# Performance work log

Hardware: AMD Instinct MI355X
Metric: run time of the kernel (lower is better)

Reference implementation:

```python
import jax, jax.numpy as jnp
import numpy as np

B, SRC = 32, 1024
SEQ_LEN, CONTEXT_LEN, D_MODEL, VOCAB = 128, 5, 512, 32000


def setup_inputs() -> dict:
    key = jax.random.key(0)
    k1, k2, k3, k4, k5, k6 = jax.random.split(key, 6)
    x = jax.random.randint(k1, (B, SRC), 0, VOCAB, dtype=jnp.int64 if jax.config.jax_enable_x64 else jnp.int32)
    yc = jax.random.randint(k2, (B, SEQ_LEN * CONTEXT_LEN), 0, VOCAB, dtype=x.dtype)
    F_emb = jax.random.normal(k3, (VOCAB, D_MODEL), dtype=jnp.float32) * 0.02
    G_emb = jax.random.normal(k4, (VOCAB, D_MODEL), dtype=jnp.float32) * 0.02
    fan_in = CONTEXT_LEN * D_MODEL
    P_w = jax.random.uniform(k5, (fan_in, D_MODEL), dtype=jnp.float32,
                             minval=-1.0, maxval=1.0) * (fan_in ** -0.5)
    P_b = jnp.zeros((D_MODEL,), dtype=jnp.float32)
    return {"x": x, "yc": yc, "F_emb": F_emb, "G_emb": G_emb, "P_w": P_w, "P_b": P_b}


def reference(x, yc, F_emb, G_emb, P_w, P_b):
    # padding mask from source tokens: 1.0 where token == 0
    mask = (x == 0).astype(jnp.float32)                      # [B, SRC]
    xe = F_emb[x]                                            # [B, SRC, D]
    yce = G_emb[yc].reshape(-1, SEQ_LEN, CONTEXT_LEN * D_MODEL)  # [B, SEQ, C*D]
    py = jnp.einsum('bsk,kd->bsd', yce, P_w) + P_b           # Dense P(y): [B, SEQ, D]
    a = jnp.einsum('bxd,bsd->bxs', xe, py)                   # [B, SRC, SEQ]
    a = a + mask[:, :, None] * -1e9                          # mask padded source rows
    a = jnp.transpose(a, (0, 2, 1))                          # [B, SEQ, SRC]
    a = jax.nn.softmax(a, axis=-1)
    out = jnp.einsum('bsx,bxd->bsd', a, xe)                  # [B, SEQ, D]
    return (out, a)
```

## Files before the change

kernel.cpp:

```cpp
#include <hip/hip_runtime.h>
#include <hip/hip_bf16.h>
#include <stdint.h>

#define BATCH 32
#define SRCN 1024
#define SEQL 128
#define CTXN 5
#define DMOD 512

typedef __attribute__((ext_vector_type(8))) short short8;
typedef __attribute__((ext_vector_type(4))) float floatx4;

typedef __attribute__((address_space(3))) void lds_t;
typedef __attribute__((address_space(1))) void glb_t;

__device__ __forceinline__ void gload_lds16(const void* g, void* l) {
    __builtin_amdgcn_global_load_lds((const glb_t*)g, (lds_t*)l, 16, 0, 0);
}

__device__ __forceinline__ ushort f2b(float f) {
    __hip_bfloat16 h = __float2bfloat16(f);
    return *reinterpret_cast<ushort*>(&h);
}

#define LSLOT(m, sg) ((((m) << 3) | ((sg) ^ ((m) & 7))) << 3)

__global__ __launch_bounds__(256) void k_prep(
    const int* __restrict__ yc, const float* __restrict__ G,
    ushort* __restrict__ yce,
    const float* __restrict__ Pw, ushort* __restrict__ Pwt)
{
    const int tid = threadIdx.x;
    if (blockIdx.x < 4096) {
        const int r = blockIdx.x;
        const int b = r >> 7, s = r & 127;
        for (int i = tid; i < 640; i += 256) {
            const int c = i >> 7;
            const int tok = yc[b * (SEQL * CTXN) + s * CTXN + c];
            const float4 v = *(const float4*)(G + (size_t)tok * DMOD + (i & 127) * 4);
            ushort4 o;
            o.x = f2b(v.x); o.y = f2b(v.y); o.z = f2b(v.z); o.w = f2b(v.w);
            *(ushort4*)(yce + (size_t)r * 2560 + i * 4) = o;
        }
    } else {
        __shared__ float t[64][68];
        const int bid = blockIdx.x - 4096;
        const int k0 = (bid % 40) * 64, n0 = (bid / 40) * 64;
        #pragma unroll
        for (int it = 0; it < 4; ++it) {
            const int c = tid + it * 256;
            const int kr = c >> 4, c4 = c & 15;
            const float4 v = *(const float4*)(Pw + (size_t)(k0 + kr) * DMOD + n0 + c4 * 4);
            t[kr][c4 * 4 + 0] = v.x; t[kr][c4 * 4 + 1] = v.y;
            t[kr][c4 * 4 + 2] = v.z; t[kr][c4 * 4 + 3] = v.w;
        }
        __syncthreads();
        #pragma unroll
        for (int it = 0; it < 2; ++it) {
            const int c = tid + it * 256;
            const int n = c >> 3, seg = c & 7;
            ushort4 o0, o1;
            o0.x = f2b(t[seg * 8 + 0][n]); o0.y = f2b(t[seg * 8 + 1][n]);
            o0.z = f2b(t[seg * 8 + 2][n]); o0.w = f2b(t[seg * 8 + 3][n]);
            o1.x = f2b(t[seg * 8 + 4][n]); o1.y = f2b(t[seg * 8 + 5][n]);
            o1.z = f2b(t[seg * 8 + 6][n]); o1.w = f2b(t[seg * 8 + 7][n]);
            ushort* dst = Pwt + (size_t)(n0 + n) * 2560 + k0 + seg * 8;
            *(ushort4*)dst = o0; *(ushort4*)(dst + 4) = o1;
        }
    }
}

__global__ __launch_bounds__(256) void k_gemm_py(
    const ushort* __restrict__ yce, const ushort* __restrict__ pwt,
    float* __restrict__ part)
{
    __shared__ ushort As[16 * 512];
    __shared__ ushort Bs[8 * 512];
    const int f = blockIdx.x;
    const int mlo = f & 7;
    const int n   = (f >> 3) & 7;
    const int mhi = (f >> 6) & 3;
    const int ks  = f >> 8;
    const int m = mlo | (mhi << 3);
    const int tid = threadIdx.x;
    const int w = tid >> 6, lane = tid & 63;
    const int l15 = lane & 15, q = lane >> 4;
    const int wm = w >> 1, wn = w & 1;
    const int m0 = m * 128, n0 = n * 64, koff = ks * 640;

    const int sr = lane >> 3;
    const int ssg = ((lane & 7) ^ sr) * 8;

    const ushort* Abase = yce + (size_t)(m0 + sr) * 2560 + koff + ssg;
    const ushort* Bbase = pwt + (size_t)(n0 + sr) * 2560 + koff + ssg;

    floatx4 acc[4][2];
    #pragma unroll
    for (int mi = 0; mi < 4; ++mi)
        #pragma unroll
        for (int ni = 0; ni < 2; ++ni)
            acc[mi][ni] = (floatx4){0.f, 0.f, 0.f, 0.f};

    for (int kk = 0; kk < 640; kk += 64) {
        __syncthreads();
        #pragma unroll
        for (int i = 0; i < 4; ++i) {
            const int cc = w * 4 + i;
            gload_lds16(Abase + (size_t)(cc * 8) * 2560 + kk, (void*)(As + cc * 512));
        }
        #pragma unroll
        for (int i = 0; i < 2; ++i) {
            const int cc = w * 2 + i;
            gload_lds16(Bbase + (size_t)(cc * 8) * 2560 + kk, (void*)(Bs + cc * 512));
        }
        __syncthreads();
        #pragma unroll
        for (int s2 = 0; s2 < 2; ++s2) {
            const int sg = s2 * 4 + q;
            short8 af[4], bf[2];
            #pragma unroll
            for (int mi = 0; mi < 4; ++mi)
                af[mi] = *(const short8*)(As + LSLOT(wm * 64 + mi * 16 + l15, sg));
            #pragma unroll
            for (int ni = 0; ni < 2; ++ni)
                bf[ni] = *(const short8*)(Bs + LSLOT(wn * 32 + ni * 16 + l15, sg));
            #pragma unroll
            for (int mi = 0; mi < 4; ++mi)
                #pragma unroll
                for (int ni = 0; ni < 2; ++ni)
                    acc[mi][ni] = __builtin_amdgcn_mfma_f32_16x16x32_bf16(
                        af[mi], bf[ni], acc[mi][ni], 0, 0, 0);
        }
    }

    float* dst = part + (size_t)ks * (4096LL * DMOD);
    #pragma unroll
    for (int ni = 0; ni < 2; ++ni) {
        const int col = n0 + wn * 32 + ni * 16 + l15;
        #pragma unroll
        for (int mi = 0; mi < 4; ++mi) {
            const int row0 = m0 + wm * 64 + mi * 16 + q * 4;
            #pragma unroll
            for (int r = 0; r < 4; ++r)
                dst[(size_t)(row0 + r) * DMOD + col] = acc[mi][ni][r];
        }
    }
}

__global__ __launch_bounds__(256) void k_red4(
    const float* __restrict__ part, const float* __restrict__ Pb,
    ushort* __restrict__ py)
{
    const long long SL = 4096LL * DMOD;
    const int i = blockIdx.x * 256 + threadIdx.x;
    const float4 a = *(const float4*)(part + (size_t)i * 4);
    const float4 b = *(const float4*)(part + SL + (size_t)i * 4);
    const float4 c = *(const float4*)(part + 2 * SL + (size_t)i * 4);
    const float4 d = *(const float4*)(part + 3 * SL + (size_t)i * 4);
    const float4 bias = *(const float4*)(Pb + ((i * 4) & 511));
    ushort4 o;
    o.x = f2b(a.x + b.x + c.x + d.x + bias.x);
    o.y = f2b(a.y + b.y + c.y + d.y + bias.y);
    o.z = f2b(a.z + b.z + c.z + d.z + bias.z);
    o.w = f2b(a.w + b.w + c.w + d.w + bias.w);
    *(ushort4*)(py + (size_t)i * 4) = o;
}

__global__ __launch_bounds__(256) void k_xe2(
    const int* __restrict__ x, const float* __restrict__ F,
    ushort* __restrict__ xe, ushort* __restrict__ xet)
{
    __shared__ ushort t[64][72];
    const int z = blockIdx.z;
    const int x0 = blockIdx.x * 64, d0 = blockIdx.y * 64;
    const int tid = threadIdx.x;
    #pragma unroll
    for (int it = 0; it < 4; ++it) {
        const int c = tid + it * 256;
        const int row = c >> 4, seg = c & 15;
        const int tok = x[z * SRCN + x0 + row];
        const float4 v = *(const float4*)(F + (size_t)tok * DMOD + d0 + seg * 4);
        ushort4 o;
        o.x = f2b(v.x); o.y = f2b(v.y); o.z = f2b(v.z); o.w = f2b(v.w);
        *(ushort4*)&t[row][seg * 4] = o;
        *(ushort4*)(xe + (size_t)(z * SRCN + x0 + row) * DMOD + d0 + seg * 4) = o;
    }
    __syncthreads();
    #pragma unroll
    for (int it = 0; it < 2; ++it) {
        const int c = tid + it * 256;
        const int d = c >> 3, seg = c & 7;
        ushort4 o0, o1;
        o0.x = t[seg * 8 + 0][d]; o0.y = t[seg * 8 + 1][d];
        o0.z = t[seg * 8 + 2][d]; o0.w = t[seg * 8 + 3][d];
        o1.x = t[seg * 8 + 4][d]; o1.y = t[seg * 8 + 5][d];
        o1.z = t[seg * 8 + 6][d]; o1.w = t[seg * 8 + 7][d];
        ushort* dst = xet + (size_t)(z * DMOD + d0 + d) * SRCN + x0 + seg * 8;
        *(ushort4*)dst = o0; *(ushort4*)(dst + 4) = o1;
    }
}

__global__ __launch_bounds__(256) void k_gemm_sc(
    const ushort* __restrict__ py, const int* __restrict__ x,
    const ushort* __restrict__ xe, float* __restrict__ a_out)
{
    __shared__ ushort As[16 * 512];
    __shared__ ushort Bs[8 * 512];
    const int f = blockIdx.x;
    const int g = f >> 3;
    const int b = ((g & 3) << 3) | (f & 7);
    const int n = g >> 2;
    const int tid = threadIdx.x;
    const int w = tid >> 6, lane = tid & 63;
    const int l15 = lane & 15, q = lane >> 4;
    const int wm = w >> 1, wn = w & 1;
    const int n0 = n * 64;

    const int sr = lane >> 3;
    const int ssg = ((lane & 7) ^ sr) * 8;

    const ushort* Abase = py + (size_t)(b * SEQL + sr) * DMOD + ssg;
    const ushort* Bbase = xe + (size_t)(b * SRCN + n0 + sr) * DMOD + ssg;

    floatx4 acc[4][2];
    #pragma unroll
    for (int mi = 0; mi < 4; ++mi)
        #pragma unroll
        for (int ni = 0; ni < 2; ++ni)
            acc[mi][ni] = (floatx4){0.f, 0.f, 0.f, 0.f};

    for (int kk = 0; kk < DMOD; kk += 64) {
        __syncthreads();
        #pragma unroll
        for (int i = 0; i < 4; ++i) {
            const int cc = w * 4 + i;
            gload_lds16(Abase + (size_t)(cc * 8) * DMOD + kk, (void*)(As + cc * 512));
        }
        #pragma unroll
        for (int i = 0; i < 2; ++i) {
            const int cc = w * 2 + i;
            gload_lds16(Bbase + (size_t)(cc * 8) * DMOD + kk, (void*)(Bs + cc * 512));
        }
        __syncthreads();
        #pragma unroll
        for (int s2 = 0; s2 < 2; ++s2) {
            const int sg = s2 * 4 + q;
            short8 af[4], bf[2];
            #pragma unroll
            for (int mi = 0; mi < 4; ++mi)
                af[mi] = *(const short8*)(As + LSLOT(wm * 64 + mi * 16 + l15, sg));
            #pragma unroll
            for (int ni = 0; ni < 2; ++ni)
                bf[ni] = *(const short8*)(Bs + LSLOT(wn * 32 + ni * 16 + l15, sg));
            #pragma unroll
            for (int mi = 0; mi < 4; ++mi)
                #pragma unroll
                for (int ni = 0; ni < 2; ++ni)
                    acc[mi][ni] = __builtin_amdgcn_mfma_f32_16x16x32_bf16(
                        af[mi], bf[ni], acc[mi][ni], 0, 0, 0);
        }
    }

    #pragma unroll
    for (int ni = 0; ni < 2; ++ni) {
        const int col = n0 + wn * 32 + ni * 16 + l15;
        const float msk = (x[b * SRCN + col] == 0) ? -1e9f : 0.0f;
        #pragma unroll
        for (int mi = 0; mi < 4; ++mi) {
            const int row0 = wm * 64 + mi * 16 + q * 4;
            #pragma unroll
            for (int r = 0; r < 4; ++r)
                a_out[((size_t)b * SEQL + row0 + r) * SRCN + col] = acc[mi][ni][r] + msk;
        }
    }
}

__global__ __launch_bounds__(256) void k_softmax(
    float* __restrict__ a, ushort* __restrict__ abf)
{
    const int row = blockIdx.x;
    float* p = a + (size_t)row * SRCN;
    ushort* pb = abf + (size_t)row * SRCN;
    const int tid = threadIdx.x;
    const int wave = tid >> 6, lane = tid & 63;

    float4 v = *(const float4*)(p + tid * 4);

    float mx = fmaxf(fmaxf(v.x, v.y), fmaxf(v.z, v.w));
    #pragma unroll
    for (int off = 32; off > 0; off >>= 1)
        mx = fmaxf(mx, __shfl_down(mx, off, 64));
    __shared__ float redm[4];
    if (lane == 0) redm[wave] = mx;
    __syncthreads();
    mx = fmaxf(fmaxf(redm[0], redm[1]), fmaxf(redm[2], redm[3]));

    const float e0 = __expf(v.x - mx);
    const float e1 = __expf(v.y - mx);
    const float e2 = __expf(v.z - mx);
    const float e3 = __expf(v.w - mx);

    float sm = e0 + e1 + e2 + e3;
    #pragma unroll
    for (int off = 32; off > 0; off >>= 1)
        sm += __shfl_down(sm, off, 64);
    __shared__ float reds[4];
    if (lane == 0) reds[wave] = sm;
    __syncthreads();
    sm = reds[0] + reds[1] + reds[2] + reds[3];

    const float inv = 1.0f / sm;
    float4 o;
    o.x = e0 * inv; o.y = e1 * inv; o.z = e2 * inv; o.w = e3 * inv;
    *(float4*)(p + tid * 4) = o;
    ushort4 ob;
    ob.x = f2b(o.x); ob.y = f2b(o.y); ob.z = f2b(o.z); ob.w = f2b(o.w);
    *(ushort4*)(pb + tid * 4) = ob;
}

__global__ __launch_bounds__(256) void k_gemm_out(
    const ushort* __restrict__ abf, const ushort* __restrict__ xet,
    float* __restrict__ outp)
{
    __shared__ ushort As[2 * 8 * 512];
    __shared__ ushort Bs[2 * 8 * 512];
    const int f = blockIdx.x;
    const int g = f >> 3;
    const int b = ((g & 3) << 3) | (f & 7);
    const int h = g >> 2;
    const int m = h & 1, n = h >> 1;
    const int tid = threadIdx.x;
    const int w = tid >> 6, lane = tid & 63;
    const int l15 = lane & 15, q = lane >> 4;
    const int wm = w >> 1, wn = w & 1;
    const int m0 = m * 64, n0 = n * 64;

    const int sr = lane >> 3;
    const int ssg = ((lane & 7) ^ sr) * 8;

    const ushort* Abase = abf + (size_t)(b * SEQL + m0 + sr) * SRCN + ssg;
    const ushort* Bbase = xet + (size_t)(b * DMOD + n0 + sr) * SRCN + ssg;

    floatx4 acc[2][2];
    #pragma unroll
    for (int mi = 0; mi < 2; ++mi)
        #pragma unroll
        for (int ni = 0; ni < 2; ++ni)
            acc[mi][ni] = (floatx4){0.f, 0.f, 0.f, 0.f};

    for (int kk = 0; kk < SRCN; kk += 128) {
        __syncthreads();
        #pragma unroll
        for (int sub = 0; sub < 2; ++sub) {
            #pragma unroll
            for (int i = 0; i < 2; ++i) {
                const int cc = w * 2 + i;
                gload_lds16(Abase + (size_t)(cc * 8) * SRCN + kk + sub * 64,
                            (void*)(As + sub * 4096 + cc * 512));
                gload_lds16(Bbase + (size_t)(cc * 8) * SRCN + kk + sub * 64,
                            (void*)(Bs + sub * 4096 + cc * 512));
            }
        }
        __syncthreads();
        #pragma unroll
        for (int sub = 0; sub < 2; ++sub) {
            #pragma unroll
            for (int s2 = 0; s2 < 2; ++s2) {
                const int sg = s2 * 4 + q;
                short8 af[2], bf[2];
                #pragma unroll
                for (int mi = 0; mi < 2; ++mi)
                    af[mi] = *(const short8*)(As + sub * 4096 + LSLOT(wm * 32 + mi * 16 + l15, sg));
                #pragma unroll
                for (int ni = 0; ni < 2; ++ni)
                    bf[ni] = *(const short8*)(Bs + sub * 4096 + LSLOT(wn * 32 + ni * 16 + l15, sg));
                #pragma unroll
                for (int mi = 0; mi < 2; ++mi)
                    #pragma unroll
                    for (int ni = 0; ni < 2; ++ni)
                        acc[mi][ni] = __builtin_amdgcn_mfma_f32_16x16x32_bf16(
                            af[mi], bf[ni], acc[mi][ni], 0, 0, 0);
            }
        }
    }

    #pragma unroll
    for (int ni = 0; ni < 2; ++ni) {
        const int col = n0 + wn * 32 + ni * 16 + l15;
        #pragma unroll
        for (int mi = 0; mi < 2; ++mi) {
            const int row0 = m0 + wm * 32 + mi * 16 + q * 4;
            #pragma unroll
            for (int r = 0; r < 4; ++r)
                outp[((size_t)b * SEQL + row0 + r) * DMOD + col] = acc[mi][ni][r];
        }
    }
}

extern "C" void kernel_launch(void* const* d_in, const int* in_sizes, int n_in,
                              void* d_out, int out_size, void* d_ws, size_t ws_size,
                              hipStream_t stream)
{
    const int*   x    = (const int*)d_in[0];
    const int*   yc   = (const int*)d_in[1];
    const float* Femb = (const float*)d_in[2];
    const float* Gemb = (const float*)d_in[3];
    const float* Pw   = (const float*)d_in[4];
    const float* Pb   = (const float*)d_in[5];

    float* out_p = (float*)d_out;
    float* a_p   = out_p + (size_t)BATCH * SEQL * DMOD;

    char* ws = (char*)d_ws;
    ushort* yce  = (ushort*)(ws);
    ushort* pwt  = (ushort*)(ws + 20971520);
    float*  part = (float*) (ws + 23592960);
    ushort* xe   = (ushort*)(ws);
    ushort* xet  = (ushort*)(ws + 33554432);
    ushort* py   = (ushort*)(ws + 67108864);
    ushort* abf  = (ushort*)(ws + 71303168);

    dim3 blk(256);
    k_prep<<<dim3(4416), blk, 0, stream>>>(yc, Gemb, yce, Pw, pwt);

    k_gemm_py<<<dim3(1024), blk, 0, stream>>>(yce, pwt, part);
    k_red4<<<dim3(2048), blk, 0, stream>>>(part, Pb, py);

    k_xe2<<<dim3(16, 8, 32), blk, 0, stream>>>(x, Femb, xe, xet);

    k_gemm_sc<<<dim3(512), blk, 0, stream>>>(py, x, xe, a_p);
    k_softmax<<<dim3(4096), blk, 0, stream>>>(a_p, abf);
    k_gemm_out<<<dim3(512), blk, 0, stream>>>(abf, xet, out_p);
}
```

Baseline: 221.4 us.

## Merge gather kernels, drop split-K partials, fuse bias into py GEMM epilogue

The xe/xet embedding gather and transpose now run in the same launch as the yce gather and Pw transpose, so one kernel covers all preprocessing. The py GEMM drops its 4-way split-K with fp32 partial buffers and the separate reduction kernel. It now computes full-K 64x64 tiles with two 64-wide K sub-slabs per barrier and adds the bias in its epilogue before converting to bf16. The aim is to cut a launch and the 32MB partial write/read traffic. In exchange each GEMM block does a longer serial K loop with a smaller tile and less reuse per block, and the workspace layout is reshuffled so abf aliases yce.

```diff
diff --git a/kernel.cpp b/kernel.cpp
--- a/kernel.cpp
+++ b/kernel.cpp
@@ -25,14 +25,18 @@
 
 #define LSLOT(m, sg) ((((m) << 3) | ((sg) ^ ((m) & 7))) << 3)
 
-__global__ __launch_bounds__(256) void k_prep(
+__global__ __launch_bounds__(256) void k_gather(
     const int* __restrict__ yc, const float* __restrict__ G,
     ushort* __restrict__ yce,
-    const float* __restrict__ Pw, ushort* __restrict__ Pwt)
-{
+    const float* __restrict__ Pw, ushort* __restrict__ Pwt,
+    const int* __restrict__ x, const float* __restrict__ F,
+    ushort* __restrict__ xe, ushort* __restrict__ xet)
+{
+    __shared__ char smem[17408];
     const int tid = threadIdx.x;
-    if (blockIdx.x < 4096) {
-        const int r = blockIdx.x;
+    const int bid = blockIdx.x;
+    if (bid < 4096) {
+        const int r = bid;
         const int b = r >> 7, s = r & 127;
         for (int i = tid; i < 640; i += 256) {
             const int c = i >> 7;
@@ -42,17 +46,17 @@
             o.x = f2b(v.x); o.y = f2b(v.y); o.z = f2b(v.z); o.w = f2b(v.w);
             *(ushort4*)(yce + (size_t)r * 2560 + i * 4) = o;
         }
-    } else {
-        __shared__ float t[64][68];
-        const int bid = blockIdx.x - 4096;
-        const int k0 = (bid % 40) * 64, n0 = (bid / 40) * 64;
+    } else if (bid < 4416) {
+        float* t = (float*)smem;
+        const int id = bid - 4096;
+        const int k0 = (id % 40) * 64, n0 = (id / 40) * 64;
         #pragma unroll
         for (int it = 0; it < 4; ++it) {
             const int c = tid + it * 256;
             const int kr = c >> 4, c4 = c & 15;
             const float4 v = *(const float4*)(Pw + (size_t)(k0 + kr) * DMOD + n0 + c4 * 4);
-            t[kr][c4 * 4 + 0] = v.x; t[kr][c4 * 4 + 1] = v.y;
-            t[kr][c4 * 4 + 2] = v.z; t[kr][c4 * 4 + 3] = v.w;
+            t[kr * 68 + c4 * 4 + 0] = v.x; t[kr * 68 + c4 * 4 + 1] = v.y;
+            t[kr * 68 + c4 * 4 + 2] = v.z; t[kr * 68 + c4 * 4 + 3] = v.w;
         }
         __syncthreads();
         #pragma unroll
@@ -60,143 +64,121 @@
             const int c = tid + it * 256;
             const int n = c >> 3, seg = c & 7;
             ushort4 o0, o1;
-            o0.x = f2b(t[seg * 8 + 0][n]); o0.y = f2b(t[seg * 8 + 1][n]);
-            o0.z = f2b(t[seg * 8 + 2][n]); o0.w = f2b(t[seg * 8 + 3][n]);
-            o1.x = f2b(t[seg * 8 + 4][n]); o1.y = f2b(t[seg * 8 + 5][n]);
-            o1.z = f2b(t[seg * 8 + 6][n]); o1.w = f2b(t[seg * 8 + 7][n]);
+            o0.x = f2b(t[(seg * 8 + 0) * 68 + n]); o0.y = f2b(t[(seg * 8 + 1) * 68 + n]);
+            o0.z = f2b(t[(seg * 8 + 2) * 68 + n]); o0.w = f2b(t[(seg * 8 + 3) * 68 + n]);
+            o1.x = f2b(t[(seg * 8 + 4) * 68 + n]); o1.y = f2b(t[(seg * 8 + 5) * 68 + n]);
+            o1.z = f2b(t[(seg * 8 + 6) * 68 + n]); o1.w = f2b(t[(seg * 8 + 7) * 68 + n]);
             ushort* dst = Pwt + (size_t)(n0 + n) * 2560 + k0 + seg * 8;
             *(ushort4*)dst = o0; *(ushort4*)(dst + 4) = o1;
         }
+    } else {
+        ushort* t = (ushort*)smem;
+        const int id = bid - 4416;
+        const int z = id >> 7;
+        const int rem = id & 127;
+        const int x0 = (rem & 15) * 64, d0 = (rem >> 4) * 64;
+        #pragma unroll
+        for (int it = 0; it < 4; ++it) {
+            const int c = tid + it * 256;
+            const int row = c >> 4, seg = c & 15;
+            const int tok = x[z * SRCN + x0 + row];
+            const float4 v = *(const float4*)(F + (size_t)tok * DMOD + d0 + seg * 4);
+            ushort4 o;
+            o.x = f2b(v.x); o.y = f2b(v.y); o.z = f2b(v.z); o.w = f2b(v.w);
+            *(ushort4*)&t[row * 72 + seg * 4] = o;
+            *(ushort4*)(xe + (size_t)(z * SRCN + x0 + row) * DMOD + d0 + seg * 4) = o;
+        }
+        __syncthreads();
+        #pragma unroll
+        for (int it = 0; it < 2; ++it) {
+            const int c = tid + it * 256;
+            const int d = c >> 3, seg = c & 7;
+            ushort4 o0, o1;
+            o0.x = t[(seg * 8 + 0) * 72 + d]; o0.y = t[(seg * 8 + 1) * 72 + d];
+            o0.z = t[(seg * 8 + 2) * 72 + d]; o0.w = t[(seg * 8 + 3) * 72 + d];
+            o1.x = t[(seg * 8 + 4) * 72 + d]; o1.y = t[(seg * 8 + 5) * 72 + d];
+            o1.z = t[(seg * 8 + 6) * 72 + d]; o1.w = t[(seg * 8 + 7) * 72 + d];
+            ushort* dst = xet + (size_t)(z * DMOD + d0 + d) * SRCN + x0 + seg * 8;
+            *(ushort4*)dst = o0; *(ushort4*)(dst + 4) = o1;
+        }
     }
 }
 
 __global__ __launch_bounds__(256) void k_gemm_py(
     const ushort* __restrict__ yce, const ushort* __restrict__ pwt,
-    float* __restrict__ part)
-{
-    __shared__ ushort As[16 * 512];
-    __shared__ ushort Bs[8 * 512];
+    const float* __restrict__ Pb, ushort* __restrict__ py)
+{
+    __shared__ ushort As[2 * 8 * 512];
+    __shared__ ushort Bs[2 * 8 * 512];
     const int f = blockIdx.x;
-    const int mlo = f & 7;
-    const int n   = (f >> 3) & 7;
-    const int mhi = (f >> 6) & 3;
-    const int ks  = f >> 8;
-    const int m = mlo | (mhi << 3);
+    const int wg = ((f & 7) << 6) | (f >> 3);
+    const int m = wg >> 3, n = wg & 7;
     const int tid = threadIdx.x;
     const int w = tid >> 6, lane = tid & 63;
     const int l15 = lane & 15, q = lane >> 4;
     const int wm = w >> 1, wn = w & 1;
-    const int m0 = m * 128, n0 = n * 64, koff = ks * 640;
+    const int m0 = m * 64, n0 = n * 64;
 
     const int sr = lane >> 3;
     const int ssg = ((lane & 7) ^ sr) * 8;
 
-    const ushort* Abase = yce + (size_t)(m0 + sr) * 2560 + koff + ssg;
-    const ushort* Bbase = pwt + (size_t)(n0 + sr) * 2560 + koff + ssg;
-
-    floatx4 acc[4][2];
-    #pragma unroll
-    for (int mi = 0; mi < 4; ++mi)
+    const ushort* Abase = yce + (size_t)(m0 + sr) * 2560 + ssg;
+    const ushort* Bbase = pwt + (size_t)(n0 + sr) * 2560 + ssg;
+
+    floatx4 acc[2][2];
+    #pragma unroll
+    for (int mi = 0; mi < 2; ++mi)
         #pragma unroll
         for (int ni = 0; ni < 2; ++ni)
             acc[mi][ni] = (floatx4){0.f, 0.f, 0.f, 0.f};
 
-    for (int kk = 0; kk < 640; kk += 64) {
-        __syncthreads();
-        #pragma unroll
-        for (int i = 0; i < 4; ++i) {
-            const int cc = w * 4 + i;
-            gload_lds16(Abase + (size_t)(cc * 8) * 2560 + kk, (void*)(As + cc * 512));
-        }
-        #pragma unroll
-        for (int i = 0; i < 2; ++i) {
-            const int cc = w * 2 + i;
-            gload_lds16(Bbase + (size_t)(cc * 8) * 2560 + kk, (void*)(Bs + cc * 512));
-        }
-        __syncthreads();
-        #pragma unroll
-        for (int s2 = 0; s2 < 2; ++s2) {
-            const int sg = s2 * 4 + q;
-            short8 af[4], bf[2];
-            #pragma unroll
-            for (int mi = 0; mi < 4; ++mi)
-                af[mi] = *(const short8*)(As + LSLOT(wm * 64 + mi * 16 + l15, sg));
-            #pragma unroll
-            for (int ni = 0; ni < 2; ++ni)
-                bf[ni] = *(const short8*)(Bs + LSLOT(wn * 32 + ni * 16 + l15, sg));
-            #pragma unroll
-            for (int mi = 0; mi < 4; ++mi)
+    for (int kk = 0; kk < 2560; kk += 128) {
+        __syncthreads();
+        #pragma unroll
+        for (int sub = 0; sub < 2; ++sub) {
+            #pragma unroll
+            for (int i = 0; i < 2; ++i) {
+                const int cc = w * 2 + i;
+                gload_lds16(Abase + (size_t)(cc * 8) * 2560 + kk + sub * 64,
+                            (void*)(As + sub * 4096 + cc * 512));
+                gload_lds16(Bbase + (size_t)(cc * 8) * 2560 + kk + sub * 64,
+                            (void*)(Bs + sub * 4096 + cc * 512));
+            }
+        }
+        __syncthreads();
+        #pragma unroll
+        for (int sub = 0; sub < 2; ++sub) {
+            #pragma unroll
+            for (int s2 = 0; s2 < 2; ++s2) {
+                const int sg = s2 * 4 + q;
+                short8 af[2], bf[2];
+                #pragma unroll
+                for (int mi = 0; mi < 2; ++mi)
+                    af[mi] = *(const short8*)(As + sub * 4096 + LSLOT(wm * 32 + mi * 16 + l15, sg));
                 #pragma unroll
                 for (int ni = 0; ni < 2; ++ni)
-                    acc[mi][ni] = __builtin_amdgcn_mfma_f32_16x16x32_bf16(
-                        af[mi], bf[ni], acc[mi][ni], 0, 0, 0);
-        }
-    }
-
-    float* dst = part + (size_t)ks * (4096LL * DMOD);
+                    bf[ni] = *(const short8*)(Bs + sub * 4096 + LSLOT(wn * 32 + ni * 16 + l15, sg));
+                #pragma unroll
+                for (int mi = 0; mi < 2; ++mi)
+                    #pragma unroll
+                    for (int ni = 0; ni < 2; ++ni)
+                        acc[mi][ni] = __builtin_amdgcn_mfma_f32_16x16x32_bf16(
+                            af[mi], bf[ni], acc[mi][ni], 0, 0, 0);
+            }
+        }
+    }
+
     #pragma unroll
     for (int ni = 0; ni < 2; ++ni) {
         const int col = n0 + wn * 32 + ni * 16 + l15;
-        #pragma unroll
-        for (int mi = 0; mi < 4; ++mi) {
-            const int row0 = m0 + wm * 64 + mi * 16 + q * 4;
+        const float bias = Pb[col];
+        #pragma unroll
+        for (int mi = 0; mi < 2; ++mi) {
+            const int row0 = m0 + wm * 32 + mi * 16 + q * 4;
             #pragma unroll
             for (int r = 0; r < 4; ++r)
-                dst[(size_t)(row0 + r) * DMOD + col] = acc[mi][ni][r];
-        }
-    }
-}
-
-__global__ __launch_bounds__(256) void k_red4(
-    const float* __restrict__ part, const float* __restrict__ Pb,
-    ushort* __restrict__ py)
-{
-    const long long SL = 4096LL * DMOD;
-    const int i = blockIdx.x * 256 + threadIdx.x;
-    const float4 a = *(const float4*)(part + (size_t)i * 4);
-    const float4 b = *(const float4*)(part + SL + (size_t)i * 4);
-    const float4 c = *(const float4*)(part + 2 * SL + (size_t)i * 4);
-    const float4 d = *(const float4*)(part + 3 * SL + (size_t)i * 4);
-    const float4 bias = *(const float4*)(Pb + ((i * 4) & 511));
-    ushort4 o;
-    o.x = f2b(a.x + b.x + c.x + d.x + bias.x);
-    o.y = f2b(a.y + b.y + c.y + d.y + bias.y);
-    o.z = f2b(a.z + b.z + c.z + d.z + bias.z);
-    o.w = f2b(a.w + b.w + c.w + d.w + bias.w);
-    *(ushort4*)(py + (size_t)i * 4) = o;
-}
-
-__global__ __launch_bounds__(256) void k_xe2(
-    const int* __restrict__ x, const float* __restrict__ F,
-    ushort* __restrict__ xe, ushort* __restrict__ xet)
-{
-    __shared__ ushort t[64][72];
-    const int z = blockIdx.z;
-    const int x0 = blockIdx.x * 64, d0 = blockIdx.y * 64;
-    const int tid = threadIdx.x;
-    #pragma unroll
-    for (int it = 0; it < 4; ++it) {
-        const int c = tid + it * 256;
-        const int row = c >> 4, seg = c & 15;
-        const int tok = x[z * SRCN + x0 + row];
-        const float4 v = *(const float4*)(F + (size_t)tok * DMOD + d0 + seg * 4);
-        ushort4 o;
-        o.x = f2b(v.x); o.y = f2b(v.y); o.z = f2b(v.z); o.w = f2b(v.w);
-        *(ushort4*)&t[row][seg * 4] = o;
-        *(ushort4*)(xe + (size_t)(z * SRCN + x0 + row) * DMOD + d0 + seg * 4) = o;
-    }
-    __syncthreads();
-    #pragma unroll
-    for (int it = 0; it < 2; ++it) {
-        const int c = tid + it * 256;
-        const int d = c >> 3, seg = c & 7;
-        ushort4 o0, o1;
-        o0.x = t[seg * 8 + 0][d]; o0.y = t[seg * 8 + 1][d];
-        o0.z = t[seg * 8 + 2][d]; o0.w = t[seg * 8 + 3][d];
-        o1.x = t[seg * 8 + 4][d]; o1.y = t[seg * 8 + 5][d];
-        o1.z = t[seg * 8 + 6][d]; o1.w = t[seg * 8 + 7][d];
-        ushort* dst = xet + (size_t)(z * DMOD + d0 + d) * SRCN + x0 + seg * 8;
-        *(ushort4*)dst = o0; *(ushort4*)(dst + 4) = o1;
+                py[(size_t)(row0 + r) * DMOD + col] = f2b(acc[mi][ni][r] + bias);
+        }
     }
 }
 
@@ -413,20 +395,16 @@
 
     char* ws = (char*)d_ws;
     ushort* yce  = (ushort*)(ws);
+    ushort* abf  = (ushort*)(ws);
     ushort* pwt  = (ushort*)(ws + 20971520);
-    float*  part = (float*) (ws + 23592960);
-    ushort* xe   = (ushort*)(ws);
-    ushort* xet  = (ushort*)(ws + 33554432);
-    ushort* py   = (ushort*)(ws + 67108864);
-    ushort* abf  = (ushort*)(ws + 71303168);
+    ushort* xe   = (ushort*)(ws + 23592960);
+    ushort* xet  = (ushort*)(ws + 57147392);
+    ushort* py   = (ushort*)(ws + 90701824);
 
     dim3 blk(256);
-    k_prep<<<dim3(4416), blk, 0, stream>>>(yc, Gemb, yce, Pw, pwt);
-
-    k_gemm_py<<<dim3(1024), blk, 0, stream>>>(yce, pwt, part);
-    k_red4<<<dim3(2048), blk, 0, stream>>>(part, Pb, py);
-
-    k_xe2<<<dim3(16, 8, 32), blk, 0, stream>>>(x, Femb, xe, xet);
+    k_gather<<<dim3(8512), blk, 0, stream>>>(yc, Gemb, yce, Pw, pwt, x, Femb, xe, xet);
+
+    k_gemm_py<<<dim3(512), blk, 0, stream>>>(yce, pwt, Pb, py);
 
     k_gemm_sc<<<dim3(512), blk, 0, stream>>>(py, x, xe, a_p);
     k_softmax<<<dim3(4096), blk, 0, stream>>>(a_p, abf);
```

Result: faster. 211.7 us (-4.4%).

## Merge xe gather into prep kernel and halve py GEMM split-K

Applied to the files above, without the earlier changes.

Folds the F-embedding gather and transpose into the same launch as the yc gather and Pw transpose, using wider 128-row tiles with an XOR-swizzled LDS layout and 16-byte transposed stores. The py GEMM goes from 4-way to 2-way split-K, which halves the partial-sum traffic and simplifies the reduction. Workspace buffers are rearranged so xe no longer aliases yce. It also adds smem token caching and odd padding for the Pw transpose. The trade-off is fewer GEMM blocks (512) and so less parallelism per launch, in exchange for less memory traffic and one fewer kernel launch.

```diff
diff --git a/kernel.cpp b/kernel.cpp
--- a/kernel.cpp
+++ b/kernel.cpp
@@ -25,34 +25,43 @@
 
 #define LSLOT(m, sg) ((((m) << 3) | ((sg) ^ ((m) & 7))) << 3)
 
-__global__ __launch_bounds__(256) void k_prep(
+#define PSTR 69
+
+__global__ __launch_bounds__(256) void k_gather(
     const int* __restrict__ yc, const float* __restrict__ G,
     ushort* __restrict__ yce,
-    const float* __restrict__ Pw, ushort* __restrict__ Pwt)
-{
+    const float* __restrict__ Pw, ushort* __restrict__ Pwt,
+    const int* __restrict__ x, const float* __restrict__ F,
+    ushort* __restrict__ xe, ushort* __restrict__ xet)
+{
+    __shared__ __align__(16) char smem[17664];
     const int tid = threadIdx.x;
-    if (blockIdx.x < 4096) {
-        const int r = blockIdx.x;
+    const int bid = blockIdx.x;
+    if (bid < 4096) {
+        int* toks = (int*)smem;
+        const int r = bid;
         const int b = r >> 7, s = r & 127;
+        if (tid < CTXN) toks[tid] = yc[b * (SEQL * CTXN) + s * CTXN + tid];
+        __syncthreads();
         for (int i = tid; i < 640; i += 256) {
             const int c = i >> 7;
-            const int tok = yc[b * (SEQL * CTXN) + s * CTXN + c];
+            const int tok = toks[c];
             const float4 v = *(const float4*)(G + (size_t)tok * DMOD + (i & 127) * 4);
             ushort4 o;
             o.x = f2b(v.x); o.y = f2b(v.y); o.z = f2b(v.z); o.w = f2b(v.w);
             *(ushort4*)(yce + (size_t)r * 2560 + i * 4) = o;
         }
-    } else {
-        __shared__ float t[64][68];
-        const int bid = blockIdx.x - 4096;
-        const int k0 = (bid % 40) * 64, n0 = (bid / 40) * 64;
+    } else if (bid < 4416) {
+        float* tf = (float*)smem;
+        const int id = bid - 4096;
+        const int k0 = (id % 40) * 64, n0 = (id / 40) * 64;
         #pragma unroll
         for (int it = 0; it < 4; ++it) {
             const int c = tid + it * 256;
             const int kr = c >> 4, c4 = c & 15;
             const float4 v = *(const float4*)(Pw + (size_t)(k0 + kr) * DMOD + n0 + c4 * 4);
-            t[kr][c4 * 4 + 0] = v.x; t[kr][c4 * 4 + 1] = v.y;
-            t[kr][c4 * 4 + 2] = v.z; t[kr][c4 * 4 + 3] = v.w;
+            tf[kr * PSTR + c4 * 4 + 0] = v.x; tf[kr * PSTR + c4 * 4 + 1] = v.y;
+            tf[kr * PSTR + c4 * 4 + 2] = v.z; tf[kr * PSTR + c4 * 4 + 3] = v.w;
         }
         __syncthreads();
         #pragma unroll
@@ -60,12 +69,45 @@
             const int c = tid + it * 256;
             const int n = c >> 3, seg = c & 7;
             ushort4 o0, o1;
-            o0.x = f2b(t[seg * 8 + 0][n]); o0.y = f2b(t[seg * 8 + 1][n]);
-            o0.z = f2b(t[seg * 8 + 2][n]); o0.w = f2b(t[seg * 8 + 3][n]);
-            o1.x = f2b(t[seg * 8 + 4][n]); o1.y = f2b(t[seg * 8 + 5][n]);
-            o1.z = f2b(t[seg * 8 + 6][n]); o1.w = f2b(t[seg * 8 + 7][n]);
+            o0.x = f2b(tf[(seg * 8 + 0) * PSTR + n]); o0.y = f2b(tf[(seg * 8 + 1) * PSTR + n]);
+            o0.z = f2b(tf[(seg * 8 + 2) * PSTR + n]); o0.w = f2b(tf[(seg * 8 + 3) * PSTR + n]);
+            o1.x = f2b(tf[(seg * 8 + 4) * PSTR + n]); o1.y = f2b(tf[(seg * 8 + 5) * PSTR + n]);
+            o1.z = f2b(tf[(seg * 8 + 6) * PSTR + n]); o1.w = f2b(tf[(seg * 8 + 7) * PSTR + n]);
             ushort* dst = Pwt + (size_t)(n0 + n) * 2560 + k0 + seg * 8;
             *(ushort4*)dst = o0; *(ushort4*)(dst + 4) = o1;
+        }
+    } else {
+        ushort* t = (ushort*)smem;
+        int* toks = (int*)(smem + 16384);
+        const int id = bid - 4416;
+        const int z = id >> 6;
+        const int rem = id & 63;
+        const int x0 = (rem & 7) * 128, d0 = (rem >> 3) * 64;
+        if (tid < 128) toks[tid] = x[z * SRCN + x0 + tid];
+        __syncthreads();
+        #pragma unroll
+        for (int it = 0; it < 8; ++it) {
+            const int c = tid + it * 256;
+            const int row = c >> 4, seg = c & 15;
+            const int tok = toks[row];
+            const float4 v = *(const float4*)(F + (size_t)tok * DMOD + d0 + seg * 4);
+            ushort4 o;
+            o.x = f2b(v.x); o.y = f2b(v.y); o.z = f2b(v.z); o.w = f2b(v.w);
+            const int sg2 = seg ^ ((row >> 3) & 15);
+            *(ushort4*)&t[row * 64 + sg2 * 4] = o;
+            *(ushort4*)(xe + (size_t)(z * SRCN + x0 + row) * DMOD + d0 + seg * 4) = o;
+        }
+        __syncthreads();
+        #pragma unroll
+        for (int it = 0; it < 4; ++it) {
+            const int c = tid + it * 256;
+            const int xs = c & 15, d = c >> 4;
+            const int sbase = ((d >> 2) ^ xs) * 4 + (d & 3);
+            short8 o;
+            #pragma unroll
+            for (int r = 0; r < 8; ++r)
+                o[r] = (short)t[(xs * 8 + r) * 64 + sbase];
+            *(short8*)(xet + (size_t)(z * DMOD + d0 + d) * SRCN + x0 + xs * 8) = o;
         }
     }
 }
@@ -77,16 +119,17 @@
     __shared__ ushort As[16 * 512];
     __shared__ ushort Bs[8 * 512];
     const int f = blockIdx.x;
-    const int mlo = f & 7;
-    const int n   = (f >> 3) & 7;
-    const int mhi = (f >> 6) & 3;
     const int ks  = f >> 8;
+    const int idx = f & 255;
+    const int mlo = idx & 7;
+    const int n   = (idx >> 3) & 7;
+    const int mhi = idx >> 6;
     const int m = mlo | (mhi << 3);
     const int tid = threadIdx.x;
     const int w = tid >> 6, lane = tid & 63;
     const int l15 = lane & 15, q = lane >> 4;
     const int wm = w >> 1, wn = w & 1;
-    const int m0 = m * 128, n0 = n * 64, koff = ks * 640;
+    const int m0 = m * 128, n0 = n * 64, koff = ks * 1280;
 
     const int sr = lane >> 3;
     const int ssg = ((lane & 7) ^ sr) * 8;
@@ -101,7 +144,7 @@
         for (int ni = 0; ni < 2; ++ni)
             acc[mi][ni] = (floatx4){0.f, 0.f, 0.f, 0.f};
 
-    for (int kk = 0; kk < 640; kk += 64) {
+    for (int kk = 0; kk < 1280; kk += 64) {
         __syncthreads();
         #pragma unroll
         for (int i = 0; i < 4; ++i) {
@@ -147,7 +190,7 @@
     }
 }
 
-__global__ __launch_bounds__(256) void k_red4(
+__global__ __launch_bounds__(256) void k_red2(
     const float* __restrict__ part, const float* __restrict__ Pb,
     ushort* __restrict__ py)
 {
@@ -155,49 +198,13 @@
     const int i = blockIdx.x * 256 + threadIdx.x;
     const float4 a = *(const float4*)(part + (size_t)i * 4);
     const float4 b = *(const float4*)(part + SL + (size_t)i * 4);
-    const float4 c = *(const float4*)(part + 2 * SL + (size_t)i * 4);
-    const float4 d = *(const float4*)(part + 3 * SL + (size_t)i * 4);
     const float4 bias = *(const float4*)(Pb + ((i * 4) & 511));
     ushort4 o;
-    o.x = f2b(a.x + b.x + c.x + d.x + bias.x);
-    o.y = f2b(a.y + b.y + c.y + d.y + bias.y);
-    o.z = f2b(a.z + b.z + c.z + d.z + bias.z);
-    o.w = f2b(a.w + b.w + c.w + d.w + bias.w);
+    o.x = f2b(a.x + b.x + bias.x);
+    o.y = f2b(a.y + b.y + bias.y);
+    o.z = f2b(a.z + b.z + bias.z);
+    o.w = f2b(a.w + b.w + bias.w);
     *(ushort4*)(py + (size_t)i * 4) = o;
-}
-
-__global__ __launch_bounds__(256) void k_xe2(
-    const int* __restrict__ x, const float* __restrict__ F,
-    ushort* __restrict__ xe, ushort* __restrict__ xet)
-{
-    __shared__ ushort t[64][72];
-    const int z = blockIdx.z;
-    const int x0 = blockIdx.x * 64, d0 = blockIdx.y * 64;
-    const int tid = threadIdx.x;
-    #pragma unroll
-    for (int it = 0; it < 4; ++it) {
-        const int c = tid + it * 256;
-        const int row = c >> 4, seg = c & 15;
-        const int tok = x[z * SRCN + x0 + row];
-        const float4 v = *(const float4*)(F + (size_t)tok * DMOD + d0 + seg * 4);
-        ushort4 o;
-        o.x = f2b(v.x); o.y = f2b(v.y); o.z = f2b(v.z); o.w = f2b(v.w);
-        *(ushort4*)&t[row][seg * 4] = o;
-        *(ushort4*)(xe + (size_t)(z * SRCN + x0 + row) * DMOD + d0 + seg * 4) = o;
-    }
-    __syncthreads();
-    #pragma unroll
-    for (int it = 0; it < 2; ++it) {
-        const int c = tid + it * 256;
-        const int d = c >> 3, seg = c & 7;
-        ushort4 o0, o1;
-        o0.x = t[seg * 8 + 0][d]; o0.y = t[seg * 8 + 1][d];
-        o0.z = t[seg * 8 + 2][d]; o0.w = t[seg * 8 + 3][d];
-        o1.x = t[seg * 8 + 4][d]; o1.y = t[seg * 8 + 5][d];
-        o1.z = t[seg * 8 + 6][d]; o1.w = t[seg * 8 + 7][d];
-        ushort* dst = xet + (size_t)(z * DMOD + d0 + d) * SRCN + x0 + seg * 8;
-        *(ushort4*)dst = o0; *(ushort4*)(dst + 4) = o1;
-    }
 }
 
 __global__ __launch_bounds__(256) void k_gemm_sc(
@@ -413,20 +420,18 @@
 
     char* ws = (char*)d_ws;
     ushort* yce  = (ushort*)(ws);
+    ushort* abf  = (ushort*)(ws);
     ushort* pwt  = (ushort*)(ws + 20971520);
-    float*  part = (float*) (ws + 23592960);
-    ushort* xe   = (ushort*)(ws);
-    ushort* xet  = (ushort*)(ws + 33554432);
-    ushort* py   = (ushort*)(ws + 67108864);
-    ushort* abf  = (ushort*)(ws + 71303168);
+    ushort* xe   = (ushort*)(ws + 23592960);
+    ushort* xet  = (ushort*)(ws + 57147392);
+    float*  part = (float*) (ws + 90701824);
+    ushort* py   = (ushort*)(ws + 107479040);
 
     dim3 blk(256);
-    k_prep<<<dim3(4416), blk, 0, stream>>>(yc, Gemb, yce, Pw, pwt);
-
-    k_gemm_py<<<dim3(1024), blk, 0, stream>>>(yce, pwt, part);
-    k_red4<<<dim3(2048), blk, 0, stream>>>(part, Pb, py);
-
-    k_xe2<<<dim3(16, 8, 32), blk, 0, stream>>>(x, Femb, xe, xet);
+    k_gather<<<dim3(6464), blk, 0, stream>>>(yc, Gemb, yce, Pw, pwt, x, Femb, xe, xet);
+
+    k_gemm_py<<<dim3(512), blk, 0, stream>>>(yce, pwt, part);
+    k_red2<<<dim3(2048), blk, 0, stream>>>(part, Pb, py);
 
     k_gemm_sc<<<dim3(512), blk, 0, stream>>>(py, x, xe, a_p);
     k_softmax<<<dim3(4096), blk, 0, stream>>>(a_p, abf);
```

After: 220.4 us. Within noise of the previous version (-0.5%).
